# Kernel optimization log

Measured on AMD Instinct MI355X. Metric: run time of the kernel, lower is better.

## Reference

```python
import jax, jax.numpy as jnp
import numpy as np
from jax import lax

CHANNELS, MID, GROUPS, PATCH = 512, 512, 8, 16
DROP_RATE = 0.1
NEG = -1e9


def setup_inputs() -> dict:
    key = jax.random.key(0)
    k0, k1, k2, k3, k4, k5 = jax.random.split(key, 6)
    B, T = 2, 8192
    x = jax.random.normal(k0, (B, CHANNELS, T), dtype=jnp.float32)
    # weight-norm conv is reparametrized plain conv; sample small weights directly
    W_qkv = jax.random.normal(k1, (3 * MID, CHANNELS // GROUPS, 5, 1), dtype=jnp.float32) * 0.05
    b_qkv = jax.random.normal(k2, (3 * MID,), dtype=jnp.float32) * 0.05
    W_out = jax.random.normal(k3, (CHANNELS, MID, 3), dtype=jnp.float32) * 0.05
    b_out = jax.random.normal(k4, (CHANNELS,), dtype=jnp.float32) * 0.05
    # bernoulli(p=dropRate) mask on k (detached in the original), shape of k
    drop_mask = (jax.random.uniform(k5, (B, MID, T // PATCH, PATCH)) < DROP_RATE).astype(jnp.float32)
    return {"x": x, "W_qkv": W_qkv, "b_qkv": b_qkv, "W_out": W_out, "b_out": b_out, "drop_mask": drop_mask}


def reference(x, W_qkv, b_qkv, W_out, b_out, drop_mask):
    B, C, T = x.shape
    pad = (-T) % PATCH  # static
    if pad:
        x = jnp.pad(x, ((0, 0), (0, 0), (0, pad)))
    wordNum = (T + pad) // PATCH
    x4 = x.reshape(B, C, wordNum, PATCH)  # [B,C,wordNum,patch]
    qkv = lax.conv_general_dilated(
        x4, W_qkv, window_strides=(1, 1), padding=[(2, 2), (0, 0)],
        dimension_numbers=("NCHW", "OIHW", "NCHW"), feature_group_count=GROUPS,
    ) + b_qkv[None, :, None, None]
    q, k, v = jnp.split(qkv, 3, axis=1)  # each [B,MID,wordNum,patch]
    k = k + drop_mask * NEG  # inline bernoulli dropout on k (mask is a constant)
    d = MID * PATCH

    def flat(t):  # [B,MID,wordNum,patch] -> [B,wordNum,MID*patch]
        return t.transpose(0, 2, 1, 3).reshape(B, wordNum, d)

    q = jax.nn.softmax(flat(q), axis=-1)   # softmax over features
    k = jax.nn.softmax(flat(k), axis=-2)   # softmax over sequence
    v = flat(v)
    kv = jnp.einsum("bki,bkj->bij", k, v)  # [B,d,d]
    out = jnp.einsum("bik,bkj->bij", q, kv)  # [B,wordNum,d]
    out = out.reshape(B, wordNum, MID, PATCH).transpose(0, 2, 1, 3).reshape(B, MID, wordNum * PATCH)
    out = lax.conv_general_dilated(
        out, W_out, window_strides=(1,), padding=[(1, 1)],
        dimension_numbers=("NCH", "OIH", "NCH"),
    ) + b_out[None, :, None]
    if pad:
        out = out[:, :, :-pad]
    return out
```

## Files before the change

### kernel.cpp

```cpp
#include <hip/hip_runtime.h>

#define CH 512
#define TT 8192
#define WN 512
#define NEGC -1000000000.0f

typedef _Float16 f16;
typedef f16 half8 __attribute__((ext_vector_type(8)));
typedef float floatx16 __attribute__((ext_vector_type(16)));

#define MFMA(a, b, c) __builtin_amdgcn_mfma_f32_32x32x16_f16(a, b, c, 0, 0, 0)

__device__ __forceinline__ half8 lds_read_frag(const f16* lds, int row, int chunk) {
    return *(const half8*)(lds + row * 64 + (((chunk ^ (row & 7))) << 3));
}
__device__ __forceinline__ void lds_write_chunk(f16* lds, int row, int chunk, half8 v) {
    *(half8*)(lds + row * 64 + ((chunk ^ (row & 7)) << 3)) = v;
}

__global__ __launch_bounds__(256) void prep_w(
    const float* __restrict__ Wq, const float* __restrict__ Wo,
    f16* __restrict__ Wq5, f16* __restrict__ Wo3)
{
    int i = blockIdx.x * 256 + threadIdx.x;
    const int NQ = 5 * 1536 * 64;
    if (i < NQ) {
        int kh = i / (1536 * 64);
        int r = i % (1536 * 64);
        int o = r >> 6, ci = r & 63;
        Wq5[i] = (f16)Wq[o * 320 + ci * 5 + kh];
    } else {
        int j = i - NQ;
        if (j < 3 * 512 * 512) {
            int kt = j / (512 * 512);
            int r = j % (512 * 512);
            int co = r >> 9, ci = r & 511;
            Wo3[j] = (f16)Wo[co * 1536 + ci * 3 + kt];
        }
    }
}

__global__ __launch_bounds__(256) void transpose_cvt(
    const float* __restrict__ src, size_t bstride, f16* __restrict__ dst)
{
    __shared__ float tl[64][65];
    int tid = threadIdx.x;
    int t0 = blockIdx.x * 64, c0 = blockIdx.y * 64, b = blockIdx.z;
    const float* sp = src + (size_t)b * bstride + (size_t)c0 * TT + t0;
#pragma unroll
    for (int i = 0; i < 16; i++) {
        int row = (tid >> 6) + i * 4;
        tl[row][tid & 63] = sp[(size_t)row * TT + (tid & 63)];
    }
    __syncthreads();
    f16* dp = dst + ((size_t)b * TT + t0) * 512 + c0;
#pragma unroll
    for (int i = 0; i < 16; i++) {
        int t = (tid >> 6) + i * 4;
        dp[(size_t)t * 512 + (tid & 63)] = (f16)tl[tid & 63][t];
    }
}

__global__ __launch_bounds__(256) void qkv_mfma(
    const f16* __restrict__ xT, const f16* __restrict__ Wq5, const float* __restrict__ bq,
    float* __restrict__ qkb, f16* __restrict__ vb16)
{
    __shared__ f16 xs[320 * 64];
    int tid = threadIdx.x;
    int b = blockIdx.x >> 5;
    int t0 = (blockIdx.x & 31) * 256;
    int m = blockIdx.y;
    int ob = m * 64;
    int g = m / 3;

    const f16* xb = xT + ((size_t)b * TT) * 512 + g * 64;
#pragma unroll
    for (int l = 0; l < 10; l++) {
        int q = tid + l * 256;
        int row = q >> 3, c16 = q & 7;
        int t = t0 - 32 + row;
        half8 v = {};
        if ((unsigned)t < (unsigned)TT) v = *(const half8*)(xb + (size_t)t * 512 + c16 * 8);
        lds_write_chunk(xs, row, c16, v);
    }
    __syncthreads();

    int wid = tid >> 6, l = tid & 63;
    int ln31 = l & 31, lhi = l >> 5;
    floatx16 acc[2][2] = {};
#pragma unroll
    for (int kh = 0; kh < 5; kh++) {
        const f16* wk = Wq5 + (size_t)kh * 1536 * 64;
#pragma unroll
        for (int ks = 0; ks < 4; ks++) {
            half8 a0 = *(const half8*)(wk + (size_t)(ob + ln31) * 64 + ks * 16 + lhi * 8);
            half8 a1 = *(const half8*)(wk + (size_t)(ob + 32 + ln31) * 64 + ks * 16 + lhi * 8);
            int chunk = ks * 2 + lhi;
            int r0 = wid * 64 + kh * 16 + ln31;
            half8 b0 = lds_read_frag(xs, r0, chunk);
            half8 b1 = lds_read_frag(xs, r0 + 32, chunk);
            acc[0][0] = MFMA(a0, b0, acc[0][0]);
            acc[0][1] = MFMA(a0, b1, acc[0][1]);
            acc[1][0] = MFMA(a1, b0, acc[1][0]);
            acc[1][1] = MFMA(a1, b1, acc[1][1]);
        }
    }
#pragma unroll
    for (int mf = 0; mf < 2; mf++)
#pragma unroll
        for (int nf = 0; nf < 2; nf++)
#pragma unroll
            for (int r = 0; r < 16; r++) {
                int o = ob + mf * 32 + (r & 3) + 8 * (r >> 2) + 4 * lhi;
                int t = t0 + wid * 64 + nf * 32 + ln31;
                float val = acc[mf][nf][r] + bq[o];
                if (o < 1024)
                    qkb[((size_t)b * 1024 + o) * TT + t] = val;
                else
                    vb16[((size_t)b * 512 + (o - 1024)) * TT + t] = (f16)val;
            }
}

__global__ __launch_bounds__(256) void softmax_q(float* __restrict__ qkb)
{
    int w = blockIdx.x, b = blockIdx.y, tid = threadIdx.x;
    float* base = qkb + (size_t)b * 1024 * TT + (size_t)w * 16;

    float val[32];
    float mx = -1e30f;
#pragma unroll
    for (int kk = 0; kk < 32; kk++) {
        int e = tid + kk * 256;
        float v = base[((size_t)(e >> 4)) * TT + (e & 15)];
        val[kk] = v;
        mx = fmaxf(mx, v);
    }
#pragma unroll
    for (int o = 32; o > 0; o >>= 1) mx = fmaxf(mx, __shfl_xor(mx, o));
    __shared__ float red[4];
    int wv = tid >> 6;
    if ((tid & 63) == 0) red[wv] = mx;
    __syncthreads();
    mx = fmaxf(fmaxf(red[0], red[1]), fmaxf(red[2], red[3]));

    float s = 0.f;
#pragma unroll
    for (int kk = 0; kk < 32; kk++) { val[kk] = __expf(val[kk] - mx); s += val[kk]; }
#pragma unroll
    for (int o = 32; o > 0; o >>= 1) s += __shfl_xor(s, o);
    __syncthreads();
    if ((tid & 63) == 0) red[wv] = s;
    __syncthreads();
    s = red[0] + red[1] + red[2] + red[3];
    float inv = 1.f / s;
#pragma unroll
    for (int kk = 0; kk < 32; kk++) {
        int e = tid + kk * 256;
        base[((size_t)(e >> 4)) * TT + (e & 15)] = val[kk] * inv;
    }
}

__global__ __launch_bounds__(256) void softmax_k(
    float* __restrict__ qkb, const float* __restrict__ mask)
{
    int c = blockIdx.x, b = blockIdx.y, tid = threadIdx.x;
    float* kp = qkb + ((size_t)(b * 1024 + 512 + c)) * TT;
    const float* mp = mask + ((size_t)(b * 512 + c)) * TT;

    float val[32];
    float mx = -1e30f;
#pragma unroll
    for (int kk = 0; kk < 32; kk++) {
        int e = tid + kk * 256;
        float v = kp[e] + mp[e] * NEGC;
        val[kk] = v;
        mx = fmaxf(mx, v);
    }
    mx = fmaxf(mx, __shfl_xor(mx, 16));
    mx = fmaxf(mx, __shfl_xor(mx, 32));
    __shared__ float red[4][16];
    int wv = tid >> 6, ln = tid & 63;
    if (ln < 16) red[wv][ln] = mx;
    __syncthreads();
    int p = tid & 15;
    mx = fmaxf(fmaxf(red[0][p], red[1][p]), fmaxf(red[2][p], red[3][p]));

    float s = 0.f;
#pragma unroll
    for (int kk = 0; kk < 32; kk++) { val[kk] = __expf(val[kk] - mx); s += val[kk]; }
    s += __shfl_xor(s, 16);
    s += __shfl_xor(s, 32);
    __syncthreads();
    if (ln < 16) red[wv][ln] = s;
    __syncthreads();
    s = red[0][p] + red[1][p] + red[2][p] + red[3][p];
    float inv = 1.f / s;
#pragma unroll
    for (int kk = 0; kk < 32; kk++)
        kp[tid + kk * 256] = val[kk] * inv;
}

__global__ __launch_bounds__(256) void vperm(
    const f16* __restrict__ vb16, f16* __restrict__ vpw)
{
    int c = blockIdx.x, b = blockIdx.y, tid = threadIdx.x;
    __shared__ f16 tl[512 * 17];
    const f16* ip = vb16 + ((size_t)b * 512 + c) * TT;
    f16* op = vpw + ((size_t)b * 512 + c) * 16 * 512;
#pragma unroll
    for (int i = 0; i < 32; i++) {
        int e = tid + i * 256;
        tl[(e >> 4) * 17 + (e & 15)] = ip[e];
    }
    __syncthreads();
#pragma unroll
    for (int i = 0; i < 32; i++) {
        int o = tid + i * 256;
        op[o] = tl[(o & 511) * 17 + (o >> 9)];
    }
}

__global__ __launch_bounds__(256) void zero_s(float* __restrict__ S)
{
    S[(size_t)blockIdx.x * 256 + threadIdx.x] = 0.f;
}

__global__ __launch_bounds__(256) void qk_mfma(
    const f16* __restrict__ qT, const f16* __restrict__ kT, float* __restrict__ S)
{
    __shared__ f16 As[128 * 64];
    __shared__ f16 Bs[128 * 64];
    int tid = threadIdx.x;
    int mt = blockIdx.x & 3, nt = blockIdx.x >> 2;
    int kz = blockIdx.y, b = blockIdx.z;
    int iw0 = mt * 128, w0 = nt * 128;
    const f16* qb_ = qT + (size_t)b * TT * 512;
    const f16* kb_ = kT + (size_t)b * TT * 512;
    int wid = tid >> 6, l = tid & 63, ln31 = l & 31, lhi = l >> 5;
    int wm = (wid >> 1) * 64, wn = (wid & 1) * 64;
    floatx16 acc[2][2] = {};

    for (int step = 0; step < 8; step++) {
        int k0 = kz * 512 + step * 64;
        int p0 = k0 >> 9, c0 = k0 & 511;
        __syncthreads();
#pragma unroll
        for (int li = 0; li < 4; li++) {
            int q = tid + li * 256;
            int row = q >> 3, c16 = q & 7;
            half8 av = *(const half8*)(qb_ + ((size_t)((iw0 + row) * 16 + p0)) * 512 + c0 + c16 * 8);
            half8 bv = *(const half8*)(kb_ + ((size_t)((w0 + row) * 16 + p0)) * 512 + c0 + c16 * 8);
            lds_write_chunk(As, row, c16, av);
            lds_write_chunk(Bs, row, c16, bv);
        }
        __syncthreads();
#pragma unroll
        for (int ks = 0; ks < 4; ks++) {
            int chunk = ks * 2 + lhi;
            half8 a0 = lds_read_frag(As, wm + ln31, chunk);
            half8 a1 = lds_read_frag(As, wm + 32 + ln31, chunk);
            half8 b0 = lds_read_frag(Bs, wn + ln31, chunk);
            half8 b1 = lds_read_frag(Bs, wn + 32 + ln31, chunk);
            acc[0][0] = MFMA(a0, b0, acc[0][0]);
            acc[0][1] = MFMA(a0, b1, acc[0][1]);
            acc[1][0] = MFMA(a1, b0, acc[1][0]);
            acc[1][1] = MFMA(a1, b1, acc[1][1]);
        }
    }
    float* Sb = S + (size_t)b * WN * WN;
#pragma unroll
    for (int mf = 0; mf < 2; mf++)
#pragma unroll
        for (int nf = 0; nf < 2; nf++)
#pragma unroll
            for (int r = 0; r < 16; r++) {
                int iw = iw0 + wm + mf * 32 + (r & 3) + 8 * (r >> 2) + 4 * lhi;
                int w = w0 + wn + nf * 32 + ln31;
                atomicAdd(&Sb[(size_t)iw * WN + w], acc[mf][nf][r]);
            }
}

__global__ __launch_bounds__(256) void sv_mfma(
    const float* __restrict__ S, const f16* __restrict__ vpw, f16* __restrict__ abufT)
{
    __shared__ f16 As[128 * 64];
    __shared__ f16 Bs[128 * 64];
    int tid = threadIdx.x;
    int mt = blockIdx.x, nt = blockIdx.y;
    int b = blockIdx.z >> 4, p = blockIdx.z & 15;
    int iw0 = mt * 128, c0n = nt * 128;
    const float* Sb = S + (size_t)b * WN * WN;
    const f16* vb_ = vpw + ((size_t)b * 512) * 16 * 512;
    int wid = tid >> 6, l = tid & 63, ln31 = l & 31, lhi = l >> 5;
    int wm = (wid >> 1) * 64, wn = (wid & 1) * 64;
    floatx16 acc[2][2] = {};

    for (int step = 0; step < 8; step++) {
        int w0k = step * 64;
        __syncthreads();
#pragma unroll
        for (int li = 0; li < 4; li++) {
            int q = tid + li * 256;
            int row = q >> 3, c16 = q & 7;
            const float* sp = Sb + (size_t)(iw0 + row) * WN + w0k + c16 * 8;
            float4 f0 = *(const float4*)(sp);
            float4 f1 = *(const float4*)(sp + 4);
            half8 av;
            av[0] = (f16)f0.x; av[1] = (f16)f0.y; av[2] = (f16)f0.z; av[3] = (f16)f0.w;
            av[4] = (f16)f1.x; av[5] = (f16)f1.y; av[6] = (f16)f1.z; av[7] = (f16)f1.w;
            half8 bv = *(const half8*)(vb_ + ((size_t)(c0n + row) * 16 + p) * 512 + w0k + c16 * 8);
            lds_write_chunk(As, row, c16, av);
            lds_write_chunk(Bs, row, c16, bv);
        }
        __syncthreads();
#pragma unroll
        for (int ks = 0; ks < 4; ks++) {
            int chunk = ks * 2 + lhi;
            half8 a0 = lds_read_frag(As, wm + ln31, chunk);
            half8 a1 = lds_read_frag(As, wm + 32 + ln31, chunk);
            half8 b0 = lds_read_frag(Bs, wn + ln31, chunk);
            half8 b1 = lds_read_frag(Bs, wn + 32 + ln31, chunk);
            acc[0][0] = MFMA(a0, b0, acc[0][0]);
            acc[0][1] = MFMA(a0, b1, acc[0][1]);
            acc[1][0] = MFMA(a1, b0, acc[1][0]);
            acc[1][1] = MFMA(a1, b1, acc[1][1]);
        }
    }
#pragma unroll
    for (int mf = 0; mf < 2; mf++)
#pragma unroll
        for (int nf = 0; nf < 2; nf++)
#pragma unroll
            for (int r = 0; r < 16; r++) {
                int iw = iw0 + wm + mf * 32 + (r & 3) + 8 * (r >> 2) + 4 * lhi;
                int c = c0n + wn + nf * 32 + ln31;
                int t = iw * 16 + p;
                abufT[((size_t)b * TT + t) * 512 + c] = (f16)acc[mf][nf][r];
            }
}

__global__ __launch_bounds__(256) void out_mfma(
    const f16* __restrict__ abufT, const f16* __restrict__ Wo3, const float* __restrict__ bo,
    float* __restrict__ out)
{
    __shared__ f16 Bs[130 * 64];
    int tid = threadIdx.x;
    int b = blockIdx.x >> 6;
    int t0 = (blockIdx.x & 63) * 128;
    int co0 = blockIdx.y * 128;
    const f16* ab = abufT + ((size_t)b * TT) * 512;
    int wid = tid >> 6, l = tid & 63, ln31 = l & 31, lhi = l >> 5;
    int wm = (wid >> 1) * 64, wn = (wid & 1) * 64;
    floatx16 acc[2][2] = {};

    for (int kc = 0; kc < 8; kc++) {
        int ci0 = kc * 64;
        __syncthreads();
#pragma unroll
        for (int li = 0; li < 5; li++) {
            int q = tid + li * 256;
            if (q < 1040) {
                int row = q >> 3, c16 = q & 7;
                int t = t0 - 1 + row;
                half8 v = {};
                if ((unsigned)t < (unsigned)TT) v = *(const half8*)(ab + (size_t)t * 512 + ci0 + c16 * 8);
                lds_write_chunk(Bs, row, c16, v);
            }
        }
        __syncthreads();
#pragma unroll
        for (int kt = 0; kt < 3; kt++) {
            const f16* wk = Wo3 + (size_t)kt * 512 * 512 + ci0;
#pragma unroll
            for (int ks = 0; ks < 4; ks++) {
                half8 a0 = *(const half8*)(wk + (size_t)(co0 + wm + ln31) * 512 + ks * 16 + lhi * 8);
                half8 a1 = *(const half8*)(wk + (size_t)(co0 + wm + 32 + ln31) * 512 + ks * 16 + lhi * 8);
                int chunk = ks * 2 + lhi;
                int r0 = wn + ln31 + kt;
                half8 b0 = lds_read_frag(Bs, r0, chunk);
                half8 b1 = lds_read_frag(Bs, r0 + 32, chunk);
                acc[0][0] = MFMA(a0, b0, acc[0][0]);
                acc[0][1] = MFMA(a0, b1, acc[0][1]);
                acc[1][0] = MFMA(a1, b0, acc[1][0]);
                acc[1][1] = MFMA(a1, b1, acc[1][1]);
            }
        }
    }
#pragma unroll
    for (int mf = 0; mf < 2; mf++)
#pragma unroll
        for (int nf = 0; nf < 2; nf++)
#pragma unroll
            for (int r = 0; r < 16; r++) {
                int co = co0 + wm + mf * 32 + (r & 3) + 8 * (r >> 2) + 4 * lhi;
                int t = t0 + wn + nf * 32 + ln31;
                out[((size_t)b * CH + co) * TT + t] = acc[mf][nf][r] + bo[co];
            }
}

extern "C" void kernel_launch(void* const* d_in, const int* in_sizes, int n_in,
                              void* d_out, int out_size, void* d_ws, size_t ws_size,
                              hipStream_t stream)
{
    const float* x    = (const float*)d_in[0];
    const float* Wq   = (const float*)d_in[1];
    const float* bq   = (const float*)d_in[2];
    const float* Wo   = (const float*)d_in[3];
    const float* bo   = (const float*)d_in[4];
    const float* mask = (const float*)d_in[5];
    float* out = (float*)d_out;
    (void)in_sizes; (void)n_in; (void)out_size; (void)ws_size;

    char* W = (char*)d_ws;
    float* qkb  = (float*)W;
    f16*   vpw  = (f16*)W;
    f16*   xT   = (f16*)(W + 67108864);
    f16*   abufT = xT;
    f16*   vb16 = (f16*)(W + 67108864 + 16777216);
    f16*   qT   = (f16*)(W + 67108864 + 2 * 16777216);
    f16*   kT   = (f16*)(W + 67108864 + 3 * 16777216);
    float* S    = (float*)(W + 67108864 + 4 * 16777216);
    f16*   Wq5  = (f16*)(W + 67108864 + 4 * 16777216 + 2097152);
    f16*   Wo3  = (f16*)(W + 67108864 + 4 * 16777216 + 2097152 + 983040);

    prep_w<<<4992, 256, 0, stream>>>(Wq, Wo, Wq5, Wo3);
    transpose_cvt<<<dim3(128, 8, 2), 256, 0, stream>>>(x, (size_t)512 * TT, xT);
    qkv_mfma<<<dim3(64, 24), 256, 0, stream>>>(xT, Wq5, bq, qkb, vb16);
    softmax_q<<<dim3(WN, 2), 256, 0, stream>>>(qkb);
    softmax_k<<<dim3(512, 2), 256, 0, stream>>>(qkb, mask);
    transpose_cvt<<<dim3(128, 8, 2), 256, 0, stream>>>(qkb, (size_t)1024 * TT, qT);
    transpose_cvt<<<dim3(128, 8, 2), 256, 0, stream>>>(qkb + (size_t)512 * TT, (size_t)1024 * TT, kT);
    vperm<<<dim3(512, 2), 256, 0, stream>>>(vb16, vpw);
    zero_s<<<2048, 256, 0, stream>>>(S);
    qk_mfma<<<dim3(16, 16, 2), 256, 0, stream>>>(qT, kT, S);
    sv_mfma<<<dim3(4, 4, 32), 256, 0, stream>>>(S, vpw, abufT);
    out_mfma<<<dim3(128, 4), 256, 0, stream>>>(abufT, Wo3, bo, out);
}
```

Before: 345.5 us.

## Store q/k in fp16, drop transposes, pre-pack weights, replace atomics with split-K reduce

q and k are now stored in fp16 by the qkv kernel, and the softmaxes read and write fp16. This halves that traffic, and the two q/k transpose kernels are gone because qk_mfma loads the channel-major layout directly. Weights are pre-packed into MFMA fragment order so each lane does one contiguous 16-byte load. The atomicAdd-based S accumulation and its zeroing kernel are replaced by per-split partial buffers plus a reduction kernel that emits fp16 S, so sv_mfma skips its conversion. The cost is lower precision for the softmax outputs and extra partial-sum traffic.

Measured after the change: 286.9 us. 17.0% less time.

```diff
diff --git a/kernel.cpp b/kernel.cpp
--- a/kernel.cpp
+++ b/kernel.cpp
@@ -1,8 +1,6 @@
 #include <hip/hip_runtime.h>
 
-#define CH 512
 #define TT 8192
-#define WN 512
 #define NEGC -1000000000.0f
 
 typedef _Float16 f16;
@@ -12,7 +10,7 @@
 #define MFMA(a, b, c) __builtin_amdgcn_mfma_f32_32x32x16_f16(a, b, c, 0, 0, 0)
 
 __device__ __forceinline__ half8 lds_read_frag(const f16* lds, int row, int chunk) {
-    return *(const half8*)(lds + row * 64 + (((chunk ^ (row & 7))) << 3));
+    return *(const half8*)(lds + row * 64 + ((chunk ^ (row & 7)) << 3));
 }
 __device__ __forceinline__ void lds_write_chunk(f16* lds, int row, int chunk, half8 v) {
     *(half8*)(lds + row * 64 + ((chunk ^ (row & 7)) << 3)) = v;
@@ -20,22 +18,29 @@
 
 __global__ __launch_bounds__(256) void prep_w(
     const float* __restrict__ Wq, const float* __restrict__ Wo,
-    f16* __restrict__ Wq5, f16* __restrict__ Wo3)
+    f16* __restrict__ WqP, f16* __restrict__ WoP)
 {
     int i = blockIdx.x * 256 + threadIdx.x;
-    const int NQ = 5 * 1536 * 64;
+    const int NQ = 48 * 5 * 4 * 512;
     if (i < NQ) {
-        int kh = i / (1536 * 64);
-        int r = i % (1536 * 64);
-        int o = r >> 6, ci = r & 63;
-        Wq5[i] = (f16)Wq[o * 320 + ci * 5 + kh];
+        int idx = i & 511, l = idx >> 3, e = idx & 7;
+        int fi = i >> 9;
+        int ks = fi & 3; fi >>= 2;
+        int kh = fi % 5; int cb = fi / 5;
+        int o = cb * 32 + (l & 31);
+        int ci = ks * 16 + (l >> 5) * 8 + e;
+        WqP[i] = (f16)Wq[o * 320 + ci * 5 + kh];
     } else {
         int j = i - NQ;
-        if (j < 3 * 512 * 512) {
-            int kt = j / (512 * 512);
-            int r = j % (512 * 512);
-            int co = r >> 9, ci = r & 511;
-            Wo3[j] = (f16)Wo[co * 1536 + ci * 3 + kt];
+        if (j < 16 * 3 * 8 * 4 * 512) {
+            int idx = j & 511, l = idx >> 3, e = idx & 7;
+            int fj = j >> 9;
+            int ks = fj & 3; fj >>= 2;
+            int kc = fj & 7; fj >>= 3;
+            int kt = fj % 3; int cb = fj / 3;
+            int co = cb * 32 + (l & 31);
+            int ci = kc * 64 + ks * 16 + (l >> 5) * 8 + e;
+            WoP[j] = (f16)Wo[co * 1536 + ci * 3 + kt];
         }
     }
 }
@@ -62,8 +67,8 @@
 }
 
 __global__ __launch_bounds__(256) void qkv_mfma(
-    const f16* __restrict__ xT, const f16* __restrict__ Wq5, const float* __restrict__ bq,
-    float* __restrict__ qkb, f16* __restrict__ vb16)
+    const f16* __restrict__ xT, const f16* __restrict__ WqP, const float* __restrict__ bq,
+    f16* __restrict__ qk16, f16* __restrict__ vb16)
 {
     __shared__ f16 xs[320 * 64];
     int tid = threadIdx.x;
@@ -75,8 +80,8 @@
 
     const f16* xb = xT + ((size_t)b * TT) * 512 + g * 64;
 #pragma unroll
-    for (int l = 0; l < 10; l++) {
-        int q = tid + l * 256;
+    for (int lp = 0; lp < 10; lp++) {
+        int q = tid + lp * 256;
         int row = q >> 3, c16 = q & 7;
         int t = t0 - 32 + row;
         half8 v = {};
@@ -90,11 +95,11 @@
     floatx16 acc[2][2] = {};
 #pragma unroll
     for (int kh = 0; kh < 5; kh++) {
-        const f16* wk = Wq5 + (size_t)kh * 1536 * 64;
 #pragma unroll
         for (int ks = 0; ks < 4; ks++) {
-            half8 a0 = *(const half8*)(wk + (size_t)(ob + ln31) * 64 + ks * 16 + lhi * 8);
-            half8 a1 = *(const half8*)(wk + (size_t)(ob + 32 + ln31) * 64 + ks * 16 + lhi * 8);
+            int fi = ((m * 2) * 5 + kh) * 4 + ks;
+            half8 a0 = *(const half8*)(WqP + (size_t)fi * 512 + l * 8);
+            half8 a1 = *(const half8*)(WqP + (size_t)(fi + 20) * 512 + l * 8);
             int chunk = ks * 2 + lhi;
             int r0 = wid * 64 + kh * 16 + ln31;
             half8 b0 = lds_read_frag(xs, r0, chunk);
@@ -115,23 +120,23 @@
                 int t = t0 + wid * 64 + nf * 32 + ln31;
                 float val = acc[mf][nf][r] + bq[o];
                 if (o < 1024)
-                    qkb[((size_t)b * 1024 + o) * TT + t] = val;
+                    qk16[((size_t)b * 1024 + o) * TT + t] = (f16)val;
                 else
                     vb16[((size_t)b * 512 + (o - 1024)) * TT + t] = (f16)val;
             }
 }
 
-__global__ __launch_bounds__(256) void softmax_q(float* __restrict__ qkb)
+__global__ __launch_bounds__(256) void softmax_q(f16* __restrict__ qk16)
 {
     int w = blockIdx.x, b = blockIdx.y, tid = threadIdx.x;
-    float* base = qkb + (size_t)b * 1024 * TT + (size_t)w * 16;
+    f16* base = qk16 + (size_t)b * 1024 * TT + (size_t)w * 16;
 
     float val[32];
     float mx = -1e30f;
 #pragma unroll
     for (int kk = 0; kk < 32; kk++) {
         int e = tid + kk * 256;
-        float v = base[((size_t)(e >> 4)) * TT + (e & 15)];
+        float v = (float)base[((size_t)(e >> 4)) * TT + (e & 15)];
         val[kk] = v;
         mx = fmaxf(mx, v);
     }
@@ -156,15 +161,15 @@
 #pragma unroll
     for (int kk = 0; kk < 32; kk++) {
         int e = tid + kk * 256;
-        base[((size_t)(e >> 4)) * TT + (e & 15)] = val[kk] * inv;
+        base[((size_t)(e >> 4)) * TT + (e & 15)] = (f16)(val[kk] * inv);
     }
 }
 
 __global__ __launch_bounds__(256) void softmax_k(
-    float* __restrict__ qkb, const float* __restrict__ mask)
+    f16* __restrict__ qk16, const float* __restrict__ mask)
 {
     int c = blockIdx.x, b = blockIdx.y, tid = threadIdx.x;
-    float* kp = qkb + ((size_t)(b * 1024 + 512 + c)) * TT;
+    f16* kp = qk16 + ((size_t)(b * 1024 + 512 + c)) * TT;
     const float* mp = mask + ((size_t)(b * 512 + c)) * TT;
 
     float val[32];
@@ -172,7 +177,7 @@
 #pragma unroll
     for (int kk = 0; kk < 32; kk++) {
         int e = tid + kk * 256;
-        float v = kp[e] + mp[e] * NEGC;
+        float v = (float)kp[e] + mp[e] * NEGC;
         val[kk] = v;
         mx = fmaxf(mx, v);
     }
@@ -197,7 +202,7 @@
     float inv = 1.f / s;
 #pragma unroll
     for (int kk = 0; kk < 32; kk++)
-        kp[tid + kk * 256] = val[kk] * inv;
+        kp[tid + kk * 256] = (f16)(val[kk] * inv);
 }
 
 __global__ __launch_bounds__(256) void vperm(
@@ -220,13 +225,8 @@
     }
 }
 
-__global__ __launch_bounds__(256) void zero_s(float* __restrict__ S)
-{
-    S[(size_t)blockIdx.x * 256 + threadIdx.x] = 0.f;
-}
-
 __global__ __launch_bounds__(256) void qk_mfma(
-    const f16* __restrict__ qT, const f16* __restrict__ kT, float* __restrict__ S)
+    const f16* __restrict__ qk16, float* __restrict__ Spart)
 {
     __shared__ f16 As[128 * 64];
     __shared__ f16 Bs[128 * 64];
@@ -234,24 +234,23 @@
     int mt = blockIdx.x & 3, nt = blockIdx.x >> 2;
     int kz = blockIdx.y, b = blockIdx.z;
     int iw0 = mt * 128, w0 = nt * 128;
-    const f16* qb_ = qT + (size_t)b * TT * 512;
-    const f16* kb_ = kT + (size_t)b * TT * 512;
+    const f16* qb_ = qk16 + (size_t)b * 1024 * TT;
+    const f16* kb_ = qb_ + (size_t)512 * TT;
     int wid = tid >> 6, l = tid & 63, ln31 = l & 31, lhi = l >> 5;
     int wm = (wid >> 1) * 64, wn = (wid & 1) * 64;
     floatx16 acc[2][2] = {};
 
     for (int step = 0; step < 8; step++) {
-        int k0 = kz * 512 + step * 64;
-        int p0 = k0 >> 9, c0 = k0 & 511;
-        __syncthreads();
-#pragma unroll
-        for (int li = 0; li < 4; li++) {
-            int q = tid + li * 256;
-            int row = q >> 3, c16 = q & 7;
-            half8 av = *(const half8*)(qb_ + ((size_t)((iw0 + row) * 16 + p0)) * 512 + c0 + c16 * 8);
-            half8 bv = *(const half8*)(kb_ + ((size_t)((w0 + row) * 16 + p0)) * 512 + c0 + c16 * 8);
-            lds_write_chunk(As, row, c16, av);
-            lds_write_chunk(Bs, row, c16, bv);
+        int c_abs = kz * 32 + step * 4 + wid;
+        __syncthreads();
+        const f16* qrow = qb_ + (size_t)c_abs * TT + iw0 * 16;
+        const f16* krow = kb_ + (size_t)c_abs * TT + w0 * 16;
+#pragma unroll
+        for (int i = 0; i < 4; i++) {
+            int j = l + i * 64;
+            int row = j >> 1, ch = wid * 2 + (j & 1);
+            lds_write_chunk(As, row, ch, *(const half8*)(qrow + j * 8));
+            lds_write_chunk(Bs, row, ch, *(const half8*)(krow + j * 8));
         }
         __syncthreads();
 #pragma unroll
@@ -267,7 +266,7 @@
             acc[1][1] = MFMA(a1, b1, acc[1][1]);
         }
     }
-    float* Sb = S + (size_t)b * WN * WN;
+    float* Sp = Spart + ((size_t)(kz * 2 + b) * 512) * 512;
 #pragma unroll
     for (int mf = 0; mf < 2; mf++)
 #pragma unroll
@@ -276,12 +275,22 @@
             for (int r = 0; r < 16; r++) {
                 int iw = iw0 + wm + mf * 32 + (r & 3) + 8 * (r >> 2) + 4 * lhi;
                 int w = w0 + wn + nf * 32 + ln31;
-                atomicAdd(&Sb[(size_t)iw * WN + w], acc[mf][nf][r]);
-            }
+                Sp[(size_t)iw * 512 + w] = acc[mf][nf][r];
+            }
+}
+
+__global__ __launch_bounds__(256) void s_reduce(
+    const float* __restrict__ Spart, f16* __restrict__ S16)
+{
+    int id = blockIdx.x * 256 + threadIdx.x;
+    float s = 0.f;
+#pragma unroll
+    for (int kz = 0; kz < 16; kz++) s += Spart[(size_t)kz * 524288 + id];
+    S16[id] = (f16)s;
 }
 
 __global__ __launch_bounds__(256) void sv_mfma(
-    const float* __restrict__ S, const f16* __restrict__ vpw, f16* __restrict__ abufT)
+    const f16* __restrict__ S16, const f16* __restrict__ vpw, f16* __restrict__ abufT)
 {
     __shared__ f16 As[128 * 64];
     __shared__ f16 Bs[128 * 64];
@@ -289,7 +298,7 @@
     int mt = blockIdx.x, nt = blockIdx.y;
     int b = blockIdx.z >> 4, p = blockIdx.z & 15;
     int iw0 = mt * 128, c0n = nt * 128;
-    const float* Sb = S + (size_t)b * WN * WN;
+    const f16* Sb = S16 + (size_t)b * 512 * 512;
     const f16* vb_ = vpw + ((size_t)b * 512) * 16 * 512;
     int wid = tid >> 6, l = tid & 63, ln31 = l & 31, lhi = l >> 5;
     int wm = (wid >> 1) * 64, wn = (wid & 1) * 64;
@@ -302,12 +311,7 @@
         for (int li = 0; li < 4; li++) {
             int q = tid + li * 256;
             int row = q >> 3, c16 = q & 7;
-            const float* sp = Sb + (size_t)(iw0 + row) * WN + w0k + c16 * 8;
-            float4 f0 = *(const float4*)(sp);
-            float4 f1 = *(const float4*)(sp + 4);
-            half8 av;
-            av[0] = (f16)f0.x; av[1] = (f16)f0.y; av[2] = (f16)f0.z; av[3] = (f16)f0.w;
-            av[4] = (f16)f1.x; av[5] = (f16)f1.y; av[6] = (f16)f1.z; av[7] = (f16)f1.w;
+            half8 av = *(const half8*)(Sb + (size_t)(iw0 + row) * 512 + w0k + c16 * 8);
             half8 bv = *(const half8*)(vb_ + ((size_t)(c0n + row) * 16 + p) * 512 + w0k + c16 * 8);
             lds_write_chunk(As, row, c16, av);
             lds_write_chunk(Bs, row, c16, bv);
@@ -340,7 +344,7 @@
 }
 
 __global__ __launch_bounds__(256) void out_mfma(
-    const f16* __restrict__ abufT, const f16* __restrict__ Wo3, const float* __restrict__ bo,
+    const f16* __restrict__ abufT, const f16* __restrict__ WoP, const float* __restrict__ bo,
     float* __restrict__ out)
 {
     __shared__ f16 Bs[130 * 64];
@@ -351,6 +355,7 @@
     const f16* ab = abufT + ((size_t)b * TT) * 512;
     int wid = tid >> 6, l = tid & 63, ln31 = l & 31, lhi = l >> 5;
     int wm = (wid >> 1) * 64, wn = (wid & 1) * 64;
+    int cb0 = blockIdx.y * 4 + (wid >> 1) * 2;
     floatx16 acc[2][2] = {};
 
     for (int kc = 0; kc < 8; kc++) {
@@ -370,11 +375,11 @@
         __syncthreads();
 #pragma unroll
         for (int kt = 0; kt < 3; kt++) {
-            const f16* wk = Wo3 + (size_t)kt * 512 * 512 + ci0;
 #pragma unroll
             for (int ks = 0; ks < 4; ks++) {
-                half8 a0 = *(const half8*)(wk + (size_t)(co0 + wm + ln31) * 512 + ks * 16 + lhi * 8);
-                half8 a1 = *(const half8*)(wk + (size_t)(co0 + wm + 32 + ln31) * 512 + ks * 16 + lhi * 8);
+                int fi = ((cb0 * 3 + kt) * 8 + kc) * 4 + ks;
+                half8 a0 = *(const half8*)(WoP + (size_t)fi * 512 + l * 8);
+                half8 a1 = *(const half8*)(WoP + (size_t)(fi + 96) * 512 + l * 8);
                 int chunk = ks * 2 + lhi;
                 int r0 = wn + ln31 + kt;
                 half8 b0 = lds_read_frag(Bs, r0, chunk);
@@ -394,7 +399,7 @@
             for (int r = 0; r < 16; r++) {
                 int co = co0 + wm + mf * 32 + (r & 3) + 8 * (r >> 2) + 4 * lhi;
                 int t = t0 + wn + nf * 32 + ln31;
-                out[((size_t)b * CH + co) * TT + t] = acc[mf][nf][r] + bo[co];
+                out[((size_t)b * 512 + co) * TT + t] = acc[mf][nf][r] + bo[co];
             }
 }
 
@@ -412,27 +417,24 @@
     (void)in_sizes; (void)n_in; (void)out_size; (void)ws_size;
 
     char* W = (char*)d_ws;
-    float* qkb  = (float*)W;
-    f16*   vpw  = (f16*)W;
-    f16*   xT   = (f16*)(W + 67108864);
+    f16*   qk16  = (f16*)W;
+    f16*   xT    = (f16*)(W + 33554432);
     f16*   abufT = xT;
-    f16*   vb16 = (f16*)(W + 67108864 + 16777216);
-    f16*   qT   = (f16*)(W + 67108864 + 2 * 16777216);
-    f16*   kT   = (f16*)(W + 67108864 + 3 * 16777216);
-    float* S    = (float*)(W + 67108864 + 4 * 16777216);
-    f16*   Wq5  = (f16*)(W + 67108864 + 4 * 16777216 + 2097152);
-    f16*   Wo3  = (f16*)(W + 67108864 + 4 * 16777216 + 2097152 + 983040);
-
-    prep_w<<<4992, 256, 0, stream>>>(Wq, Wo, Wq5, Wo3);
+    f16*   vb16  = (f16*)(W + 50331648);
+    f16*   vpw   = (f16*)(W + 67108864);
+    float* Spart = (float*)(W + 83886080);
+    f16*   S16   = (f16*)(W + 117440512);
+    f16*   WqP   = (f16*)(W + 118489088);
+    f16*   WoP   = (f16*)(W + 119472128);
+
+    prep_w<<<4992, 256, 0, stream>>>(Wq, Wo, WqP, WoP);
     transpose_cvt<<<dim3(128, 8, 2), 256, 0, stream>>>(x, (size_t)512 * TT, xT);
-    qkv_mfma<<<dim3(64, 24), 256, 0, stream>>>(xT, Wq5, bq, qkb, vb16);
-    softmax_q<<<dim3(WN, 2), 256, 0, stream>>>(qkb);
-    softmax_k<<<dim3(512, 2), 256, 0, stream>>>(qkb, mask);
-    transpose_cvt<<<dim3(128, 8, 2), 256, 0, stream>>>(qkb, (size_t)1024 * TT, qT);
-    transpose_cvt<<<dim3(128, 8, 2), 256, 0, stream>>>(qkb + (size_t)512 * TT, (size_t)1024 * TT, kT);
+    qkv_mfma<<<dim3(64, 24), 256, 0, stream>>>(xT, WqP, bq, qk16, vb16);
+    softmax_q<<<dim3(512, 2), 256, 0, stream>>>(qk16);
+    softmax_k<<<dim3(512, 2), 256, 0, stream>>>(qk16, mask);
     vperm<<<dim3(512, 2), 256, 0, stream>>>(vb16, vpw);
-    zero_s<<<2048, 256, 0, stream>>>(S);
-    qk_mfma<<<dim3(16, 16, 2), 256, 0, stream>>>(qT, kT, S);
-    sv_mfma<<<dim3(4, 4, 32), 256, 0, stream>>>(S, vpw, abufT);
-    out_mfma<<<dim3(128, 4), 256, 0, stream>>>(abufT, Wo3, bo, out);
-}
+    qk_mfma<<<dim3(16, 16, 2), 256, 0, stream>>>(qk16, Spart);
+    s_reduce<<<2048, 256, 0, stream>>>(Spart, S16);
+    sv_mfma<<<dim3(4, 4, 32), 256, 0, stream>>>(S16, vpw, abufT);
+    out_mfma<<<dim3(128, 4), 256, 0, stream>>>(abufT, WoP, bo, out);
+}
```
